# Optimization experiments

Hardware: AMD Instinct MI355X
Metric: run time of the kernel (lower is better)

The kernel has to match this reference:

```python
import jax, jax.numpy as jnp
import numpy as np

B, T, S, D, V = 32, 2048, 256, 1024, 56
STAR_PENALTY = -1.0
NEG = -1e30  # -inf surrogate that is safe for gradients


def setup_inputs() -> dict:
    key = jax.random.key(0)
    k1, k2, k3 = jax.random.split(key, 3)
    features = jax.random.normal(k1, (B, T, D), jnp.float32)
    targets = jax.random.randint(k2, (B, S), 1, V)  # 0 is the blank; labels in [1, V)
    W = jax.random.normal(k3, (V, D), jnp.float32) * (1.0 / 32.0)  # 1/sqrt(D)
    b = jnp.zeros((V,), jnp.float32)
    input_lengths = jnp.full((B,), T, jnp.int32)
    target_lengths = jnp.full((B,), S, jnp.int32)
    return dict(features=features, W=W, b=b, targets=targets,
                input_lengths=input_lengths, target_lengths=target_lengths)


def _star_ctc_losses(logp, targets, input_lengths, target_lengths, star_penalty):
    """Star-CTC forward (DP) score.
    logp: (T, N, C) log-softmax emissions; targets: (N, S) labels (blank=0 excluded).
    Extended state sequence [*, t1, *, t2, ..., tS, *]: star states play the role of
    CTC blanks but act as penalized wildcards, emitting logsumexp(logp)+star_penalty
    (== star_penalty for normalized log-probs). Standard CTC transition topology:
    self-loop, advance by 1, advance by 2 into a token state when it differs from the
    previous token. Returns per-sequence negative log-likelihood, shape (N,)."""
    Tlen, N, C = logp.shape
    Slen = targets.shape[1]
    L = 2 * Slen + 1
    ext = jnp.zeros((N, L), targets.dtype).at[:, 1::2].set(targets)  # (N, L)
    is_star = (jnp.arange(L) % 2 == 0)[None, :]                      # (1, L)
    prev2 = jnp.pad(ext[:, :-2], ((0, 0), (2, 0)), constant_values=-1)
    allow_skip = (~is_star) & (ext != prev2)                         # (N, L)

    def emit(logp_t):  # logp_t: (N, C) -> (N, L)
        star_e = star_penalty + jax.nn.logsumexp(logp_t, axis=-1, keepdims=True)
        tok_e = jnp.take_along_axis(logp_t, ext, axis=-1)
        return jnp.where(is_star, star_e, tok_e)

    alpha0 = jnp.where(jnp.arange(L)[None, :] < 2, emit(logp[0]), NEG)

    def step(alpha, xs):
        logp_t, t = xs
        a1 = jnp.pad(alpha[:, :-1], ((0, 0), (1, 0)), constant_values=NEG)
        a2 = jnp.where(allow_skip,
                       jnp.pad(alpha[:, :-2], ((0, 0), (2, 0)), constant_values=NEG),
                       NEG)
        new = jnp.logaddexp(jnp.logaddexp(alpha, a1), a2) + emit(logp_t)
        new = jnp.where(t < input_lengths[:, None], new, alpha)  # freeze past input_length
        return new, None

    alpha, _ = jax.lax.scan(step, alpha0, (logp[1:], jnp.arange(1, Tlen)))
    last = 2 * target_lengths                  # index of the final star state
    rows = jnp.arange(N)
    score = jnp.logaddexp(alpha[rows, last], alpha[rows, last - 1])
    return -score


def reference(features, W, b, targets, input_lengths, target_lengths):
    # classifier + log_softmax (Dropout(0.2) is identity at eval time)
    logits = jnp.einsum('btd,vd->btv', features, W) + b
    logp = jax.nn.log_softmax(logits.astype(jnp.float32), axis=-1)
    logp = jnp.transpose(logp, (1, 0, 2))      # (T, N, C) as in logits.permute(1,0,2)
    losses = _star_ctc_losses(logp, targets, input_lengths, target_lengths, STAR_PENALTY)
    # ctc_reduce_mean: length-normalized mean loss
    return jnp.mean(losses / target_lengths.astype(losses.dtype))
```

## Files before the change

### kernel.cpp

```cpp
#include <hip/hip_runtime.h>
#include <hip/hip_bf16.h>
#include <math.h>

typedef __attribute__((ext_vector_type(4))) float f32x4;
typedef __attribute__((ext_vector_type(8))) short s16x8;

#define LOG2E 1.4426950408889634f
#define LN2f  0.6931471805599453f
#define INV_E 0.36787944117144233f

__device__ __forceinline__ short bfc(float x) {
  unsigned u = __float_as_uint(x);
  unsigned r = u + 0x7fffu + ((u >> 16) & 1u);
  return (short)(r >> 16);
}

__device__ __forceinline__ unsigned pk2(float x, float y) {
  union { __hip_bfloat162 h; unsigned u; } c;
  c.h = __float22bfloat162_rn(make_float2(x, y));
  return c.u;
}

__device__ __forceinline__ float rdlane(float v, int lane) {
  return __int_as_float(__builtin_amdgcn_readlane(__float_as_int(v), lane));
}

__device__ __forceinline__ float pick9(int j, float a0, float a1, float a2,
                                       float a3, float a4, float a5, float a6,
                                       float a7, float a8) {
  float v = a0;
  if (j == 1) v = a1;
  if (j == 2) v = a2;
  if (j == 3) v = a3;
  if (j == 4) v = a4;
  if (j == 5) v = a5;
  if (j == 6) v = a6;
  if (j == 7) v = a7;
  if (j == 8) v = a8;
  return v;
}

__global__ void conv_w(const float* __restrict__ W, short* __restrict__ Wb,
                       int V, int D, int* __restrict__ flags, int nflags) {
  int idx = blockIdx.x * blockDim.x + threadIdx.x;
  if (idx < nflags) flags[idx] = 0;
  if (idx >= 64 * D) return;
  int row = idx / D, col = idx - row * D;
  Wb[idx] = (row < V) ? bfc(W[(size_t)row * D + col]) : (short)0;
}

__global__ __launch_bounds__(256, 2) void fused_gemm_star(
    const float* __restrict__ feat, const short* __restrict__ Wb,
    const float* __restrict__ bias, float* __restrict__ ptg,
    float* __restrict__ skb, int* __restrict__ flags,
    const int* __restrict__ targets, const int* __restrict__ in_len,
    const int* __restrict__ tgt_len, float* __restrict__ partial,
    int nrows, int D, int V, int T, int S, int B, int CPB) {

  __shared__ float gbuf[4][4][64];

  if ((int)blockIdx.x >= B) {
    const int j = blockIdx.x - B;
    const int c = j / B;
    const int b = j - c * B;
    const int tc0 = c * 128;
    const int rlen = (T - tc0 < 128) ? (T - tc0) : 128;
    const int rowlim = b * T + tc0 + rlen;

    const int lane = threadIdx.x & 63;
    const int wave = threadIdx.x >> 6;
    const int m_lo = lane & 15;
    const int q = lane >> 4;
    const size_t bstr = (size_t)16 * D;
    const int rowbase = b * T + tc0 + wave * 32;

    const int* tg = targets + (size_t)b * S;
    const int l0 = lane * 4;
    const int g1 = (l0 < S) ? tg[l0] : 0;
    const int g3 = (l0 + 1 < S) ? tg[l0 + 1] : 0;
    const int g5 = (l0 + 2 < S) ? tg[l0 + 2] : 0;
    const int g7 = (l0 + 3 < S) ? tg[l0 + 3] : 0;

    int arow0 = rowbase + m_lo;
    int arow1 = rowbase + 16 + m_lo;
    if (arow0 >= nrows) arow0 = nrows - 1;
    if (arow1 >= nrows) arow1 = nrows - 1;
    const float* A0base = feat + (size_t)arow0 * D + q * 8;
    const float* A1base = feat + (size_t)arow1 * D + q * 8;
    const short* Bbase = Wb + (size_t)m_lo * D + q * 8;

    f32x4 acc[2][4];
    #pragma unroll
    for (int g = 0; g < 2; ++g)
      #pragma unroll
      for (int ni = 0; ni < 4; ++ni) acc[g][ni] = (f32x4){0.f, 0.f, 0.f, 0.f};

#define DECLS(s) float4 al0_##s, ah0_##s, al1_##s, ah1_##s;                  \
                 s16x8 b0_##s, b1_##s, b2_##s, b3_##s
    DECLS(0); DECLS(1); DECLS(2); DECLS(3);
#undef DECLS

#define LOADS(s, kk)                                                         \
  do {                                                                       \
    const float* A0p = A0base + (kk);                                        \
    const float* A1p = A1base + (kk);                                        \
    const short* Bpp = Bbase + (kk);                                         \
    al0_##s = *(const float4*)(A0p);                                         \
    ah0_##s = *(const float4*)(A0p + 4);                                     \
    al1_##s = *(const float4*)(A1p);                                         \
    ah1_##s = *(const float4*)(A1p + 4);                                     \
    b0_##s = *(const s16x8*)(Bpp);                                           \
    b1_##s = *(const s16x8*)(Bpp + bstr);                                    \
    b2_##s = *(const s16x8*)(Bpp + 2 * bstr);                                \
    b3_##s = *(const s16x8*)(Bpp + 3 * bstr);                                \
  } while (0)

#define COMPUTE(s)                                                           \
  do {                                                                       \
    union { s16x8 v; unsigned u[4]; } av0, av1;                              \
    av0.u[0] = pk2(al0_##s.x, al0_##s.y);                                    \
    av0.u[1] = pk2(al0_##s.z, al0_##s.w);                                    \
    av0.u[2] = pk2(ah0_##s.x, ah0_##s.y);                                    \
    av0.u[3] = pk2(ah0_##s.z, ah0_##s.w);                                    \
    av1.u[0] = pk2(al1_##s.x, al1_##s.y);                                    \
    av1.u[1] = pk2(al1_##s.z, al1_##s.w);                                    \
    av1.u[2] = pk2(ah1_##s.x, ah1_##s.y);                                    \
    av1.u[3] = pk2(ah1_##s.z, ah1_##s.w);                                    \
    acc[0][0] = __builtin_amdgcn_mfma_f32_16x16x32_bf16(av0.v, b0_##s, acc[0][0], 0, 0, 0); \
    acc[0][1] = __builtin_amdgcn_mfma_f32_16x16x32_bf16(av0.v, b1_##s, acc[0][1], 0, 0, 0); \
    acc[0][2] = __builtin_amdgcn_mfma_f32_16x16x32_bf16(av0.v, b2_##s, acc[0][2], 0, 0, 0); \
    acc[0][3] = __builtin_amdgcn_mfma_f32_16x16x32_bf16(av0.v, b3_##s, acc[0][3], 0, 0, 0); \
    acc[1][0] = __builtin_amdgcn_mfma_f32_16x16x32_bf16(av1.v, b0_##s, acc[1][0], 0, 0, 0); \
    acc[1][1] = __builtin_amdgcn_mfma_f32_16x16x32_bf16(av1.v, b1_##s, acc[1][1], 0, 0, 0); \
    acc[1][2] = __builtin_amdgcn_mfma_f32_16x16x32_bf16(av1.v, b2_##s, acc[1][2], 0, 0, 0); \
    acc[1][3] = __builtin_amdgcn_mfma_f32_16x16x32_bf16(av1.v, b3_##s, acc[1][3], 0, 0, 0); \
  } while (0)

    LOADS(0, 0); LOADS(1, 32); LOADS(2, 64); LOADS(3, 96);
    for (int k0 = 0; k0 < D; k0 += 128) {
      { COMPUTE(0); int kp = k0 + 128; if (kp >= D) kp = 0;  LOADS(0, kp); }
      { COMPUTE(1); int kp = k0 + 160; if (kp >= D) kp = 32; LOADS(1, kp); }
      { COMPUTE(2); int kp = k0 + 192; if (kp >= D) kp = 64; LOADS(2, kp); }
      { COMPUTE(3); int kp = k0 + 224; if (kp >= D) kp = 96; LOADS(3, kp); }
    }
#undef LOADS
#undef COMPUTE

    float bias_v[4];
    #pragma unroll
    for (int ni = 0; ni < 4; ++ni) {
      int col = ni * 16 + m_lo;
      bias_v[ni] = (col < V) ? bias[col] : 0.f;
    }

    #pragma unroll
    for (int g = 0; g < 2; ++g) {
      #pragma unroll
      for (int r = 0; r < 4; ++r) {
        float lg[4];
        #pragma unroll
        for (int ni = 0; ni < 4; ++ni) {
          int col = ni * 16 + m_lo;
          lg[ni] = (col < V) ? (acc[g][ni][r] + bias_v[ni]) : -1e30f;
        }
        float m = fmaxf(fmaxf(lg[0], lg[1]), fmaxf(lg[2], lg[3]));
        #pragma unroll
        for (int off = 1; off < 16; off <<= 1) m = fmaxf(m, __shfl_xor(m, off));
        float p[4];
        #pragma unroll
        for (int ni = 0; ni < 4; ++ni) p[ni] = exp2f((lg[ni] - m) * LOG2E);
        float s = (p[0] + p[1]) + (p[2] + p[3]);
        #pragma unroll
        for (int off = 1; off < 16; off <<= 1) s += __shfl_xor(s, off);

        #pragma unroll
        for (int ni = 0; ni < 4; ++ni)
          gbuf[wave][q][ni * 16 + m_lo] = p[ni];

        #pragma unroll
        for (int rr = 0; rr < 4; ++rr) {
          int grow = rowbase + g * 16 + rr * 4 + r;
          if (grow < rowlim) {
            float srow = rdlane(s, rr * 16);
            float4 ev;
            ev.x = gbuf[wave][rr][g1];
            ev.y = gbuf[wave][rr][g3];
            ev.z = gbuf[wave][rr][g5];
            ev.w = gbuf[wave][rr][g7];
            *(float4*)(ptg + ((size_t)grow * 64 + lane) * 4) = ev;
            if (lane == 0) {
              float2 skv;
              skv.x = srow * INV_E;
              skv.y = logf(srow);
              *(float2*)(skb + (size_t)grow * 2) = skv;
            }
          }
        }
      }
    }

    __syncthreads();
    if (threadIdx.x == 0)
      __hip_atomic_store(&flags[b * CPB + c], 1, __ATOMIC_RELEASE,
                         __HIP_MEMORY_SCOPE_AGENT);
    return;
  }

  if (threadIdx.x >= 64) return;
  const int n = blockIdx.x;
  const int lane = threadIdx.x;
  const int len = in_len[n];
  const int tl = tgt_len[n];
  const int* tg = targets + (size_t)n * S;
  const int* fl = flags + n * CPB;
  const float* prow = ptg + (size_t)n * T * 256;
  const float* srow = skb + (size_t)n * T * 2;

  int cdone = -1;
#define WAITC(cc)                                                            \
  do {                                                                       \
    int _c = (cc);                                                           \
    if (cdone < _c) {                                                        \
      while (cdone < _c) {                                                   \
        if (__hip_atomic_load((int*)&fl[cdone + 1], __ATOMIC_RELAXED,        \
                              __HIP_MEMORY_SCOPE_AGENT))                     \
          ++cdone;                                                           \
        else                                                                 \
          __builtin_amdgcn_s_sleep(8);                                       \
      }                                                                      \
      __builtin_amdgcn_fence(__ATOMIC_ACQUIRE, "agent");                     \
    }                                                                        \
  } while (0)

  const int s0 = lane * 4;
  int lab1 = (s0     < S) ? tg[s0]     : 0;
  int lab3 = (s0 + 1 < S) ? tg[s0 + 1] : 0;
  int lab5 = (s0 + 2 < S) ? tg[s0 + 2] : 0;
  int lab7 = (s0 + 3 < S) ? tg[s0 + 3] : 0;
  int labm1 = __shfl_up(lab7, 1);
  int labm3 = __shfl_up(lab5, 1);
  const bool sk1 = (lane > 0) && (lab1 != labm1);
  const bool sk3 = (lab3 != lab1);
  const bool sk5 = (lab5 != lab3);
  const bool sk7 = (lab7 != lab5);
  const bool skm1 = (labm1 != labm3);

  float a0 = 0, a1 = 0, a2 = 0, a3 = 0, a4 = 0, a5 = 0, a6 = 0, a7 = 0, a8 = 0;
  float m1 = 0.f, m2 = 0.f, m3 = 0.f;
  int eps = 0, eL = 0;
  bool act = (lane == 0);

#define PTGL(t) (*(const float4*)(prow +                                     \
    ((size_t)(((t) < len) ? (t) : (len - 1)) * 256 + lane * 4)))
#define SKLL(t) (*(const float2*)(srow +                                     \
    ((size_t)(((t) < len) ? (t) : (len - 1)) * 2)))

  WAITC(0);

  float4 r0 = PTGL(0);
  float2 k0v = SKLL(0);
  if (lane == 0) { a0 = k0v.x; a1 = r0.x; }
  float ksum = k0v.y;

  float4 rr0 = PTGL(1), rr1 = PTGL(2), rr2 = PTGL(3), rr3 = PTGL(4);
  float4 rr4 = PTGL(5), rr5 = PTGL(6), rr6 = PTGL(7), rr7 = PTGL(8);
  float2 kr0 = SKLL(1), kr1 = SKLL(2), kr2 = SKLL(3), kr3 = SKLL(4);
  float2 kr4 = SKLL(5), kr5 = SKLL(6), kr6 = SKLL(7), kr7 = SKLL(8);

  float em1a = __shfl_up(rr0.w, 1);

#define RENORM()                                                             \
  do {                                                                       \
    float mx = fmaxf(fmaxf(fmaxf(a0, a1), fmaxf(a2, a3)),                    \
                     fmaxf(fmaxf(a4, a5), fmaxf(a6, a7)));                   \
    mx = fmaxf(mx, a8);                                                      \
    int e = (int)((__float_as_uint(mx) >> 23) & 255) - 126;                  \
    e = (act && mx > 0.f) ? e : 0;                                           \
    a0 = ldexpf(a0, -e); a1 = ldexpf(a1, -e); a2 = ldexpf(a2, -e);           \
    a3 = ldexpf(a3, -e); a4 = ldexpf(a4, -e); a5 = ldexpf(a5, -e);           \
    a6 = ldexpf(a6, -e); a7 = ldexpf(a7, -e); a8 = ldexpf(a8, -e);           \
    eps += e;                                                                \
  } while (0)

#define PAIR(EC0, EC1, KC0, KC1, NX, P0, P1, DOREN)                          \
  do {                                                                       \
    ksum += KC0.y; ksum += KC1.y;                                            \
    if (!act) eps = eL;                                                      \
    bool inc = (lane != 0) &&                                                \
               ((m1 != 0.f) || (m2 != 0.f) || (m3 != 0.f));                  \
    int d = inc ? (eL - eps) : 0;                                            \
    if (__builtin_expect(d > 24, 0)) {                  \
      a0 = ldexpf(a0, -d); a1 = ldexpf(a1, -d); a2 = ldexpf(a2, -d);         \
      a3 = ldexpf(a3, -d); a4 = ldexpf(a4, -d); a5 = ldexpf(a5, -d);         \
      a6 = ldexpf(a6, -d); a7 = ldexpf(a7, -d); a8 = ldexpf(a8, -d);         \
      eps += d;                                      \
    } else {                                                                 \
      m1 = ldexpf(m1, d); m2 = ldexpf(m2, d); m3 = ldexpf(m3, d);            \
    }                                                                        \
    act = act || (m1 != 0.f) || (m2 != 0.f) || (m3 != 0.f);                  \
                  \
    a8 = (a8 + a7) * KC0.x;                                                  \
    a7 = (a7 + a6 + (sk7 ? a5 : 0.f)) * EC0.w;                               \
    a6 = (a6 + a5) * KC0.x;                                                  \
    a5 = (a5 + a4 + (sk5 ? a3 : 0.f)) * EC0.z;                               \
    a4 = (a4 + a3) * KC0.x;                                                  \
    a3 = (a3 + a2 + (sk3 ? a1 : 0.f)) * EC0.y;                               \
    a2 = (a2 + a1) * KC0.x;                                                  \
    a1 = (a1 + a0 + (sk1 ? m1 : 0.f)) * EC0.x;                               \
    a0 = (a0 + m1) * KC0.x;                                                  \
    m1 = (m1 + m2 + (skm1 ? m3 : 0.f)) * em1a;                               \
                                                             \
    a8 = (a8 + a7) * KC1.x;                                                  \
    a7 = (a7 + a6 + (sk7 ? a5 : 0.f)) * EC1.w;                               \
    a6 = (a6 + a5) * KC1.x;                                                  \
    a5 = (a5 + a4 + (sk5 ? a3 : 0.f)) * EC1.z;                               \
    a4 = (a4 + a3) * KC1.x;                                                  \
    a3 = (a3 + a2 + (sk3 ? a1 : 0.f)) * EC1.y;                               \
    a2 = (a2 + a1) * KC1.x;                                                  \
    a1 = (a1 + a0 + (sk1 ? m1 : 0.f)) * EC1.x;                               \
    a0 = (a0 + m1) * KC1.x;                                                  \
    EC0 = PTGL(P0); EC1 = PTGL(P1);                   \
    KC0 = SKLL(P0); KC1 = SKLL(P1);                                          \
    if (DOREN) RENORM();                                                     \
    em1a = __shfl_up(NX.w, 1);                     \
                          \
    m3 = __shfl_up(a5, 1); m2 = __shfl_up(a6, 1); m1 = __shfl_up(a7, 1);     \
    eL = __shfl_up(eps, 1);                                                  \
    if (lane == 0) { m1 = 0.f; m2 = 0.f; m3 = 0.f; }                         \
  } while (0)

  int t0 = 1;
  for (; t0 + 8 <= len; t0 += 8) {
    int tmax = t0 + 15;
    if (tmax > len - 1) tmax = len - 1;
    WAITC(tmax >> 7);
    PAIR(rr0, rr1, kr0, kr1, rr2, t0 + 8,  t0 + 9,  false);
    PAIR(rr2, rr3, kr2, kr3, rr4, t0 + 10, t0 + 11, false);
    PAIR(rr4, rr5, kr4, kr5, rr6, t0 + 12, t0 + 13, false);
    PAIR(rr6, rr7, kr6, kr7, rr0, t0 + 14, t0 + 15, true);
  }

  WAITC((len - 1) >> 7);

  for (int t = t0; t < len; ++t) {
    float4 cv = PTGL(t);
    float2 kc = SKLL(t);
    ksum += kc.y;
    if (!act) eps = eL;
    bool inc = (lane != 0) && (m1 != 0.f);
    int d = inc ? (eL - eps) : 0;
    float m1s;
    if (__builtin_expect(d > 24, 0)) {
      a0 = ldexpf(a0, -d); a1 = ldexpf(a1, -d); a2 = ldexpf(a2, -d);
      a3 = ldexpf(a3, -d); a4 = ldexpf(a4, -d); a5 = ldexpf(a5, -d);
      a6 = ldexpf(a6, -d); a7 = ldexpf(a7, -d); a8 = ldexpf(a8, -d);
      eps += d; m1s = m1;
    } else {
      m1s = inc ? ldexpf(m1, d) : 0.f;
    }
    act = act || (m1s != 0.f);
    a8 = (a8 + a7) * kc.x;
    a7 = (a7 + a6 + (sk7 ? a5 : 0.f)) * cv.w;
    a6 = (a6 + a5) * kc.x;
    a5 = (a5 + a4 + (sk5 ? a3 : 0.f)) * cv.z;
    a4 = (a4 + a3) * kc.x;
    a3 = (a3 + a2 + (sk3 ? a1 : 0.f)) * cv.y;
    a2 = (a2 + a1) * kc.x;
    a1 = (a1 + a0 + (sk1 ? m1s : 0.f)) * cv.x;
    a0 = (a0 + m1s) * kc.x;
    if ((t & 7) == 0) RENORM();
    m1 = __shfl_up(a7, 1);
    eL = __shfl_up(eps, 1);
    if (lane == 0) m1 = 0.f;
  }

  int last = 2 * tl;
  int kx = last >> 3, jx = last & 7;
  if (kx > 63) { kx = 63; jx = last - 504; }
  int ky = (last - 1) >> 3, jy = (last - 1) & 7;
  float vx = pick9(jx, a0, a1, a2, a3, a4, a5, a6, a7, a8);
  float vy = pick9(jy, a0, a1, a2, a3, a4, a5, a6, a7, a8);
  float sx = __shfl(vx, kx); int ex = __shfl(eps, kx);
  float sy = __shfl(vy, ky); int ey = __shfl(eps, ky);
  if (lane == 0) {
    int em = (ex > ey) ? ex : ey;
    float v = ldexpf(sx, ex - em) + ldexpf(sy, ey - em);
    float score = logf(v) + (float)em * LN2f - ksum;
    partial[n] = -score / (float)tl;
  }
#undef WAITC
#undef PTGL
#undef SKLL
#undef RENORM
#undef PAIR
}

__global__ void reduce_mean(const float* __restrict__ partial,
                            float* __restrict__ out, int B) {
  float v = 0.f;
  for (int i = threadIdx.x; i < B; i += 64) v += partial[i];
  #pragma unroll
  for (int off = 32; off > 0; off >>= 1) v += __shfl_down(v, off, 64);
  if (threadIdx.x == 0) out[0] = v / (float)B;
}

extern "C" void kernel_launch(void* const* d_in, const int* in_sizes, int n_in,
                              void* d_out, int out_size, void* d_ws, size_t ws_size,
                              hipStream_t stream) {
  const float* feat = (const float*)d_in[0];
  const float* W = (const float*)d_in[1];
  const float* bias = (const float*)d_in[2];
  const int* targets = (const int*)d_in[3];
  const int* in_len = (const int*)d_in[4];
  const int* tgt_len = (const int*)d_in[5];
  float* out = (float*)d_out;

  const int V = in_sizes[2];
  const int D = in_sizes[1] / V;
  const int B = in_sizes[4];
  const int T = in_sizes[0] / (B * D);
  const int S = in_sizes[3] / B;
  const int nrows = B * T;

  float* ptg = (float*)d_ws;
  float* skb = ptg + (size_t)nrows * 256;
  float* partial = skb + (size_t)nrows * 2;
  short* Wb = (short*)(partial + B);
  const int CPB = (T + 127) / 128;
  int* flags = (int*)((char*)Wb + (size_t)64 * D * sizeof(short));

  conv_w<<<(64 * D + 255) / 256, 256, 0, stream>>>(W, Wb, V, D,
                                                   flags, B * CPB);

  const int NTILES = B * CPB;
  fused_gemm_star<<<dim3(B + NTILES), 256, 0, stream>>>(
      feat, Wb, bias, ptg, skb, flags, targets, in_len, tgt_len, partial,
      nrows, D, V, T, S, B, CPB);

  reduce_mean<<<1, 64, 0, stream>>>(partial, out, B);
}
```

Measured before the change: 760.3 us.

## Stage DP emission rows into an LDS ring via async global-to-LDS loads

The serial star-CTC DP wave no longer reads emission and skip rows from global memory into registers. It prefetches them 24–32 timesteps ahead into a 32-row LDS ring buffer using global_load_lds, with vmcnt waits. The goal is to hide global load latency on the latency-bound recurrence and to free the registers that held the eight-row lookahead. The cost is manual waitcnt bookkeeping. There is also a possible ordering hazard, since the LDS ring is read with no barrier or LDS wait after the vmcnt waits.

```diff
diff --git a/kernel.cpp b/kernel.cpp
--- a/kernel.cpp
+++ b/kernel.cpp
@@ -40,6 +40,12 @@
   return v;
 }
 
+__device__ __forceinline__ void gload_lds16(const float* g, float* l) {
+  __builtin_amdgcn_global_load_lds(
+      (const __attribute__((address_space(1))) unsigned int*)g,
+      (__attribute__((address_space(3))) unsigned int*)l, 16, 0, 0);
+}
+
 __global__ void conv_w(const float* __restrict__ W, short* __restrict__ Wb,
                        int V, int D, int* __restrict__ flags, int nflags) {
   int idx = blockIdx.x * blockDim.x + threadIdx.x;
@@ -57,9 +63,11 @@
     const int* __restrict__ tgt_len, float* __restrict__ partial,
     int nrows, int D, int V, int T, int S, int B, int CPB) {
 
-  __shared__ float gbuf[4][4][64];
+  __shared__ __align__(16) char smem[36864];
 
   if ((int)blockIdx.x >= B) {
+    typedef float GB[4][64];
+    GB* gbuf = (GB*)smem;
     const int j = blockIdx.x - B;
     const int c = j / B;
     const int b = j - c * B;
@@ -216,6 +224,9 @@
   const float* prow = ptg + (size_t)n * T * 256;
   const float* srow = skb + (size_t)n * T * 2;
 
+  float* ring = (float*)smem;
+  float* sklr = (float*)(smem + 32768);
+
   int cdone = -1;
 #define WAITC(cc)                                                            \
   do {                                                                       \
@@ -231,6 +242,19 @@
       __builtin_amdgcn_fence(__ATOMIC_ACQUIRE, "agent");                     \
     }                                                                        \
   } while (0)
+
+#define STAGE_ROW(t)                                                         \
+  do {                                                                       \
+    int _tt = ((t) < len) ? (t) : (len - 1);                                 \
+    gload_lds16(prow + ((size_t)_tt << 8) + (lane << 2),                     \
+                ring + (((t) & 31) << 8));                                   \
+  } while (0)
+
+#define STAGE_SK(c)                                                          \
+  gload_lds16(srow + ((size_t)(c) << 8) + (lane << 2),                       \
+              sklr + (((c) & 3) << 8))
+
+#define EROW(t) (*(const float4*)(ring + (((t) & 31) << 8) + (lane << 2)))
 
   const int s0 = lane * 4;
   int lab1 = (s0     < S) ? tg[s0]     : 0;
@@ -250,24 +274,24 @@
   int eps = 0, eL = 0;
   bool act = (lane == 0);
 
-#define PTGL(t) (*(const float4*)(prow +                                     \
-    ((size_t)(((t) < len) ? (t) : (len - 1)) * 256 + lane * 4)))
-#define SKLL(t) (*(const float2*)(srow +                                     \
-    ((size_t)(((t) < len) ? (t) : (len - 1)) * 2)))
+  #define KROW(t) krowf(sklr, (t), len)
+  struct KR { __device__ static float2 f(const float* sklr, int t, int len) {
+    int tt = (t < len) ? t : (len - 1);
+    return *(const float2*)(sklr + (((tt >> 7) & 3) << 8) + ((tt & 127) << 1));
+  } };
+  #undef KROW
+#define KROW(t) KR::f(sklr, (t), len)
 
   WAITC(0);
-
-  float4 r0 = PTGL(0);
-  float2 k0v = SKLL(0);
-  if (lane == 0) { a0 = k0v.x; a1 = r0.x; }
-  float ksum = k0v.y;
-
-  float4 rr0 = PTGL(1), rr1 = PTGL(2), rr2 = PTGL(3), rr3 = PTGL(4);
-  float4 rr4 = PTGL(5), rr5 = PTGL(6), rr6 = PTGL(7), rr7 = PTGL(8);
-  float2 kr0 = SKLL(1), kr1 = SKLL(2), kr2 = SKLL(3), kr3 = SKLL(4);
-  float2 kr4 = SKLL(5), kr5 = SKLL(6), kr6 = SKLL(7), kr7 = SKLL(8);
-
-  float em1a = __shfl_up(rr0.w, 1);
+  STAGE_SK(0);
+  #pragma unroll
+  for (int t = 0; t < 24; ++t) STAGE_ROW(t);
+  asm volatile("s_waitcnt vmcnt(0)" ::: "memory");
+
+  float4 r0v = EROW(0);
+  float2 q0v = KROW(0);
+  if (lane == 0) { a0 = q0v.x; a1 = r0v.x; }
+  float ksum = q0v.y;
 
 #define RENORM()                                                             \
   do {                                                                       \
@@ -282,9 +306,10 @@
     eps += e;                                                                \
   } while (0)
 
-#define PAIR(EC0, EC1, KC0, KC1, NX, P0, P1, DOREN)                          \
-  do {                                                                       \
-    ksum += KC0.y; ksum += KC1.y;                                            \
+#define PAIR(EA, EB, KA, KB, DOREN)                                          \
+  do {                                                                       \
+    float em1a = __shfl_up(EA.w, 1);                                         \
+    ksum += KA.y; ksum += KB.y;                                              \
     if (!act) eps = eL;                                                      \
     bool inc = (lane != 0) &&                                                \
                ((m1 != 0.f) || (m2 != 0.f) || (m3 != 0.f));                  \
@@ -299,52 +324,74 @@
     }                                                                        \
     act = act || (m1 != 0.f) || (m2 != 0.f) || (m3 != 0.f);                  \
                   \
-    a8 = (a8 + a7) * KC0.x;                                                  \
-    a7 = (a7 + a6 + (sk7 ? a5 : 0.f)) * EC0.w;                               \
-    a6 = (a6 + a5) * KC0.x;                                                  \
-    a5 = (a5 + a4 + (sk5 ? a3 : 0.f)) * EC0.z;                               \
-    a4 = (a4 + a3) * KC0.x;                                                  \
-    a3 = (a3 + a2 + (sk3 ? a1 : 0.f)) * EC0.y;                               \
-    a2 = (a2 + a1) * KC0.x;                                                  \
-    a1 = (a1 + a0 + (sk1 ? m1 : 0.f)) * EC0.x;                               \
-    a0 = (a0 + m1) * KC0.x;                                                  \
+    a8 = (a8 + a7) * KA.x;                                                   \
+    a7 = (a7 + a6 + (sk7 ? a5 : 0.f)) * EA.w;                                \
+    a6 = (a6 + a5) * KA.x;                                                   \
+    a5 = (a5 + a4 + (sk5 ? a3 : 0.f)) * EA.z;                                \
+    a4 = (a4 + a3) * KA.x;                                                   \
+    a3 = (a3 + a2 + (sk3 ? a1 : 0.f)) * EA.y;                                \
+    a2 = (a2 + a1) * KA.x;                                                   \
+    a1 = (a1 + a0 + (sk1 ? m1 : 0.f)) * EA.x;                                \
+    a0 = (a0 + m1) * KA.x;                                                   \
     m1 = (m1 + m2 + (skm1 ? m3 : 0.f)) * em1a;                               \
                                                              \
-    a8 = (a8 + a7) * KC1.x;                                                  \
-    a7 = (a7 + a6 + (sk7 ? a5 : 0.f)) * EC1.w;                               \
-    a6 = (a6 + a5) * KC1.x;                                                  \
-    a5 = (a5 + a4 + (sk5 ? a3 : 0.f)) * EC1.z;                               \
-    a4 = (a4 + a3) * KC1.x;                                                  \
-    a3 = (a3 + a2 + (sk3 ? a1 : 0.f)) * EC1.y;                               \
-    a2 = (a2 + a1) * KC1.x;                                                  \
-    a1 = (a1 + a0 + (sk1 ? m1 : 0.f)) * EC1.x;                               \
-    a0 = (a0 + m1) * KC1.x;                                                  \
-    EC0 = PTGL(P0); EC1 = PTGL(P1);                   \
-    KC0 = SKLL(P0); KC1 = SKLL(P1);                                          \
+    a8 = (a8 + a7) * KB.x;                                                   \
+    a7 = (a7 + a6 + (sk7 ? a5 : 0.f)) * EB.w;                                \
+    a6 = (a6 + a5) * KB.x;                                                   \
+    a5 = (a5 + a4 + (sk5 ? a3 : 0.f)) * EB.z;                                \
+    a4 = (a4 + a3) * KB.x;                                                   \
+    a3 = (a3 + a2 + (sk3 ? a1 : 0.f)) * EB.y;                                \
+    a2 = (a2 + a1) * KB.x;                                                   \
+    a1 = (a1 + a0 + (sk1 ? m1 : 0.f)) * EB.x;                                \
+    a0 = (a0 + m1) * KB.x;                                                   \
     if (DOREN) RENORM();                                                     \
-    em1a = __shfl_up(NX.w, 1);                     \
-                          \
     m3 = __shfl_up(a5, 1); m2 = __shfl_up(a6, 1); m1 = __shfl_up(a7, 1);     \
     eL = __shfl_up(eps, 1);                                                  \
     if (lane == 0) { m1 = 0.f; m2 = 0.f; m3 = 0.f; }                         \
   } while (0)
 
-  int t0 = 1;
+  int t0 = 1, cstage = 0;
   for (; t0 + 8 <= len; t0 += 8) {
-    int tmax = t0 + 15;
-    if (tmax > len - 1) tmax = len - 1;
-    WAITC(tmax >> 7);
-    PAIR(rr0, rr1, kr0, kr1, rr2, t0 + 8,  t0 + 9,  false);
-    PAIR(rr2, rr3, kr2, kr3, rr4, t0 + 10, t0 + 11, false);
-    PAIR(rr4, rr5, kr4, kr5, rr6, t0 + 12, t0 + 13, false);
-    PAIR(rr6, rr7, kr6, kr7, rr0, t0 + 14, t0 + 15, true);
+    int tg2 = t0 + 31; if (tg2 > len - 1) tg2 = len - 1;
+    int cg = tg2 >> 7;
+    if (cg > cdone) {
+      WAITC(cg);
+      for (int cc = cstage + 1; cc <= cg; ++cc) STAGE_SK(cc);
+      cstage = cg;
+      asm volatile("s_waitcnt vmcnt(0)" ::: "memory");
+    }
+    STAGE_ROW(t0 + 24); STAGE_ROW(t0 + 25);
+    STAGE_ROW(t0 + 26); STAGE_ROW(t0 + 27);
+    STAGE_ROW(t0 + 28); STAGE_ROW(t0 + 29);
+    STAGE_ROW(t0 + 30); STAGE_ROW(t0 + 31);
+    asm volatile("s_waitcnt vmcnt(24)" ::: "memory");
+    float4 E0 = EROW(t0),     E1 = EROW(t0 + 1);
+    float4 E2 = EROW(t0 + 2), E3 = EROW(t0 + 3);
+    float4 E4 = EROW(t0 + 4), E5 = EROW(t0 + 5);
+    float4 E6 = EROW(t0 + 6), E7 = EROW(t0 + 7);
+    float2 Q0 = KROW(t0),     Q1 = KROW(t0 + 1);
+    float2 Q2 = KROW(t0 + 2), Q3 = KROW(t0 + 3);
+    float2 Q4 = KROW(t0 + 4), Q5 = KROW(t0 + 5);
+    float2 Q6 = KROW(t0 + 6), Q7 = KROW(t0 + 7);
+    PAIR(E0, E1, Q0, Q1, false);
+    PAIR(E2, E3, Q2, Q3, false);
+    PAIR(E4, E5, Q4, Q5, false);
+    PAIR(E6, E7, Q6, Q7, true);
   }
 
-  WAITC((len - 1) >> 7);
+  {
+    int cg = (len - 1) >> 7;
+    if (cg > cdone) {
+      WAITC(cg);
+      for (int cc = cstage + 1; cc <= cg; ++cc) STAGE_SK(cc);
+      cstage = cg;
+    }
+  }
+  asm volatile("s_waitcnt vmcnt(0)" ::: "memory");
 
   for (int t = t0; t < len; ++t) {
-    float4 cv = PTGL(t);
-    float2 kc = SKLL(t);
+    float4 cv = EROW(t);
+    float2 kc = KROW(t);
     ksum += kc.y;
     if (!act) eps = eL;
     bool inc = (lane != 0) && (m1 != 0.f);
@@ -389,8 +436,10 @@
     partial[n] = -score / (float)tl;
   }
 #undef WAITC
-#undef PTGL
-#undef SKLL
+#undef STAGE_ROW
+#undef STAGE_SK
+#undef EROW
+#undef KROW
 #undef RENORM
 #undef PAIR
 }
```

New measurement: 828.2 us. +8.9%, slower.
